# Optimization experiments

Measured on AMD Instinct MI355X. Metric: run time of the kernel, lower is better.

The kernel has to match this reference:

```python
import jax, jax.numpy as jnp
import numpy as np
import math

NUM_LAYERS = 2
D_MODEL = 512
NUM_HEADS = 8
DFF = 2048
TIME_DIM = 8
B = 8
L = 512


def _ffn2(t, w1, b1, w2, b2):
    # gsm_ffn: two Dense(time_dim) layers, both with relu
    h = jax.nn.relu(t @ w1 + b1)
    return jax.nn.relu(h @ w2 + b2)


def _layer_norm(x, g, b, eps=1e-6):
    m = jnp.mean(x, axis=-1, keepdims=True)
    v = jnp.mean(jnp.square(x - m), axis=-1, keepdims=True)
    return (x - m) / jnp.sqrt(v + eps) * g + b


def _forward(x, t, wq, bq, wk, bk, wv, bv, wo, bo, w1, b1, w2, b2,
             ln1g, ln1b, ln2g, ln2b, pw1, pb1, pw2, pb2,
             sw1, sb1, sw2, sb2, bw1, bb1, bw2, bb2):
    Bn, Ln, D = x.shape
    H = NUM_HEADS
    dh = D // H
    scale = jnp.sqrt(jnp.float32(dh))
    two_pi = jnp.float32(2.0 * math.pi)
    for i in range(NUM_LAYERS):
        # ---- TimeGSMKernel: Gibbs spectral-mixture time kernel [B,L,L] ----
        pv = _ffn2(t, pw1[i], pb1[i], pw2[i], pb2[i])            # [B,L,td]
        tp = two_pi * pv * t                                      # [B,L,td]
        cos_enc = jnp.cos(tp[:, :, None, :] - tp[:, None, :, :])  # [B,L,L,td]
        sg = _ffn2(t, sw1[i], sb1[i], sw2[i], sb2[i]) + 1e-6      # [B,L,td]
        sq = sg[:, :, None, :]                                    # [B,L,1,td]
        sk = sg[:, None, :, :]                                    # [B,1,L,td]
        denom = sq * sq + sk * sk
        diff = t[:, :, None, :] - t[:, None, :, :]                # [B,L,L,1]
        exp_enc = jnp.exp(-(diff * diff) / denom)                 # [B,L,L,td]
        local_enc = jnp.sqrt(2.0 * sq * sk / denom)
        be = _ffn2(t, bw1[i], bb1[i], bw2[i], bb2[i])             # [B,L,td]
        kern = jnp.sum(be[:, :, None, :] * be[:, None, :, :]
                       * local_enc * exp_enc * cos_enc, axis=-1)  # [B,L,L]

        # ---- multi-head self-attention with kernel bias ----
        def heads(z):
            return z.reshape(Bn, Ln, H, dh).transpose(0, 2, 1, 3)
        q = heads(x @ wq[i] + bq[i])
        k = heads(x @ wk[i] + bk[i])
        v = heads(x @ wv[i] + bv[i])
        logits = jnp.einsum('bhqd,bhkd->bhqk', q, k) / scale
        logits = logits + (kern / jnp.exp(scale))[:, None, :, :]
        aw = jax.nn.softmax(logits, axis=-1)
        ctx = jnp.einsum('bhqk,bhkd->bhqd', aw, v)
        ctx = ctx.transpose(0, 2, 1, 3).reshape(Bn, Ln, D)
        attn_out = ctx @ wo[i] + bo[i]
        x = _layer_norm(x + attn_out, ln1g[i], ln1b[i])
        # ---- pointwise FFN (relu then linear) ----
        f = jax.nn.relu(x @ w1[i] + b1[i]) @ w2[i] + b2[i]
        x = _layer_norm(x + f, ln2g[i], ln2b[i])
    return x


def setup_inputs() -> dict:
    key = jax.random.key(0)
    ks = iter(jax.random.split(key, 40))
    def nrm(shape, s=0.02):
        return (jax.random.normal(next(ks), shape) * s).astype(jnp.float32)
    NL, D, TD = NUM_LAYERS, D_MODEL, TIME_DIM
    d = {
        'x': jax.random.normal(next(ks), (B, L, D), dtype=jnp.float32),
        't': jax.random.uniform(next(ks), (B, L, 1), dtype=jnp.float32),
        'wq': nrm((NL, D, D)), 'bq': jnp.zeros((NL, D), jnp.float32),
        'wk': nrm((NL, D, D)), 'bk': jnp.zeros((NL, D), jnp.float32),
        'wv': nrm((NL, D, D)), 'bv': jnp.zeros((NL, D), jnp.float32),
        'wo': nrm((NL, D, D)), 'bo': jnp.zeros((NL, D), jnp.float32),
        'w1': nrm((NL, D, DFF)), 'b1': jnp.zeros((NL, DFF), jnp.float32),
        'w2': nrm((NL, DFF, D)), 'b2': jnp.zeros((NL, D), jnp.float32),
        'ln1g': jnp.ones((NL, D), jnp.float32), 'ln1b': jnp.zeros((NL, D), jnp.float32),
        'ln2g': jnp.ones((NL, D), jnp.float32), 'ln2b': jnp.zeros((NL, D), jnp.float32),
        'pw1': nrm((NL, 1, TD), 0.5), 'pb1': 0.1 * jnp.ones((NL, TD), jnp.float32),
        'pw2': nrm((NL, TD, TD), 0.3), 'pb2': 0.1 * jnp.ones((NL, TD), jnp.float32),
        'sw1': nrm((NL, 1, TD), 0.5), 'sb1': 0.1 * jnp.ones((NL, TD), jnp.float32),
        'sw2': nrm((NL, TD, TD), 0.3), 'sb2': 0.5 * jnp.ones((NL, TD), jnp.float32),
        'bw1': nrm((NL, 1, TD), 0.5), 'bb1': 0.1 * jnp.ones((NL, TD), jnp.float32),
        'bw2': nrm((NL, TD, TD), 0.3), 'bb2': 0.1 * jnp.ones((NL, TD), jnp.float32),
    }
    return d


def reference(x, t, wq, bq, wk, bk, wv, bv, wo, bo, w1, b1, w2, b2,
              ln1g, ln1b, ln2g, ln2b, pw1, pb1, pw2, pb2,
              sw1, sb1, sw2, sb2, bw1, bb1, bw2, bb2):
    return _forward(x, t, wq, bq, wk, bk, wv, bv, wo, bo, w1, b1, w2, b2,
                    ln1g, ln1b, ln2g, ln2b, pw1, pb1, pw2, pb2,
                    sw1, sb1, sw2, sb2, bw1, bb1, bw2, bb2)
```

## Files before the change

### kernel.cpp

```cpp
#include <hip/hip_runtime.h>
#include <hip/hip_bf16.h>

#define DEV_INLINE __device__ __forceinline__

constexpr int NLAYERS = 2;
constexpr int DM = 512;
constexpr int NH = 8;
constexpr int DHD = 64;
constexpr int FF = 2048;
constexpr int TD = 8;
constexpr int BB = 8;
constexpr int LL = 512;
constexpr int ROWS = BB * LL;
constexpr int QKVN = 3 * DM;

constexpr float TWO_PI_F = 6.28318530717958647692f;
constexpr float INV_E8 = 3.3546262790251185e-4f;

typedef __attribute__((ext_vector_type(8))) short short8v;
typedef __attribute__((ext_vector_type(4))) float f32x4;

DEV_INLINE unsigned short bf16_rne(float x) {
  unsigned int u = __float_as_uint(x);
  unsigned int r = (u + 0x7fffu + ((u >> 16) & 1u)) >> 16;
  return (unsigned short)r;
}
DEV_INLINE float bf16_to_f(unsigned short h) {
  return __uint_as_float(((unsigned int)h) << 16);
}
DEV_INLINE void split_bf16(float x, unsigned short& h, unsigned short& l) {
  h = bf16_rne(x);
  float lo = x - bf16_to_f(h);
  l = bf16_rne(lo);
}

DEV_INLINE void ffn2_small(float tv,
                           const float* __restrict__ w1, const float* __restrict__ b1,
                           const float* __restrict__ w2, const float* __restrict__ b2,
                           float* out) {
  float h[TD];
#pragma unroll
  for (int d = 0; d < TD; ++d) h[d] = fmaxf(tv * w1[d] + b1[d], 0.f);
#pragma unroll
  for (int j = 0; j < TD; ++j) {
    float acc = b2[j];
#pragma unroll
    for (int d = 0; d < TD; ++d) acc += h[d] * w2[d * TD + j];
    out[j] = fmaxf(acc, 0.f);
  }
}

__global__ __launch_bounds__(256) void small_ffn_kernel(
    const float* __restrict__ t,
    const float* __restrict__ pw1, const float* __restrict__ pb1,
    const float* __restrict__ pw2, const float* __restrict__ pb2,
    const float* __restrict__ sw1, const float* __restrict__ sb1,
    const float* __restrict__ sw2, const float* __restrict__ sb2,
    const float* __restrict__ bw1, const float* __restrict__ bb1,
    const float* __restrict__ bw2, const float* __restrict__ bb2,
    float* __restrict__ tp, float* __restrict__ sg, float* __restrict__ be) {
  const int i = blockIdx.x * 256 + threadIdx.x;
  if (i >= ROWS) return;
  const float tv = t[i];
  float o[TD];
  ffn2_small(tv, pw1, pb1, pw2, pb2, o);
#pragma unroll
  for (int d = 0; d < TD; ++d) tp[(size_t)i * TD + d] = TWO_PI_F * o[d] * tv;
  ffn2_small(tv, sw1, sb1, sw2, sb2, o);
#pragma unroll
  for (int d = 0; d < TD; ++d) sg[(size_t)i * TD + d] = o[d] + 1e-6f;
  ffn2_small(tv, bw1, bb1, bw2, bb2, o);
#pragma unroll
  for (int d = 0; d < TD; ++d) be[(size_t)i * TD + d] = o[d];
}

DEV_INLINE void load8(const float* __restrict__ p, float* o) {
  float4 a = *reinterpret_cast<const float4*>(p);
  float4 b = *reinterpret_cast<const float4*>(p + 4);
  o[0] = a.x; o[1] = a.y; o[2] = a.z; o[3] = a.w;
  o[4] = b.x; o[5] = b.y; o[6] = b.z; o[7] = b.w;
}

__global__ __launch_bounds__(256) void kern_kernel(
    const float* __restrict__ t, const float* __restrict__ tp,
    const float* __restrict__ sg, const float* __restrict__ be,
    float* __restrict__ kernS) {
  const int k = blockIdx.x * 256 + threadIdx.x;
  const int q = blockIdx.y;
  const int b = blockIdx.z;
  const size_t iq = (size_t)b * LL + q;
  const size_t ik = (size_t)b * LL + k;
  const float tq = t[iq], tk = t[ik];
  const float diff = tq - tk;
  const float d2 = diff * diff;

  float tpq[TD], sgq[TD], beq[TD], tpk[TD], sgk[TD], bek[TD];
  load8(tp + iq * TD, tpq);
  load8(sg + iq * TD, sgq);
  load8(be + iq * TD, beq);
  load8(tp + ik * TD, tpk);
  load8(sg + ik * TD, sgk);
  load8(be + ik * TD, bek);

  float acc = 0.f;
#pragma unroll
  for (int d = 0; d < TD; ++d) {
    const float sq = sgq[d], sk = sgk[d];
    const float denom = sq * sq + sk * sk;
    const float inv = 1.0f / denom;
    const float e = __expf(-d2 * inv);
    const float loc = sqrtf(2.0f * sq * sk * inv);
    const float c = __cosf(tpq[d] - tpk[d]);
    acc += beq[d] * bek[d] * loc * e * c;
  }
  kernS[((size_t)b * LL + q) * LL + k] = acc * INV_E8;
}

__global__ __launch_bounds__(256) void td_kernel(
    const float* __restrict__ W, unsigned short* __restrict__ Thi,
    unsigned short* __restrict__ Tlo, int K, int N) {
  __shared__ float tile[32][33];
  const int k0 = blockIdx.x * 32, n0 = blockIdx.y * 32;
  const int tx = threadIdx.x & 31, ty = threadIdx.x >> 5;
#pragma unroll
  for (int i = 0; i < 4; ++i)
    tile[ty + i * 8][tx] = W[(size_t)(k0 + ty + i * 8) * N + n0 + tx];
  __syncthreads();
#pragma unroll
  for (int i = 0; i < 4; ++i) {
    const int n = n0 + ty + i * 8;
    const float v = tile[tx][ty + i * 8];
    unsigned short h, l;
    split_bf16(v, h, l);
    Thi[(size_t)n * K + k0 + tx] = h;
    Tlo[(size_t)n * K + k0 + tx] = l;
  }
}

__global__ __launch_bounds__(256) void decomp_kernel(
    const float* __restrict__ X, unsigned short* __restrict__ Hi,
    unsigned short* __restrict__ Lo, int n4) {
  const int i = blockIdx.x * 256 + threadIdx.x;
  if (i >= n4) return;
  const float4 v = *reinterpret_cast<const float4*>(X + (size_t)i * 4);
  unsigned short h0, h1, h2, h3, l0, l1, l2, l3;
  split_bf16(v.x, h0, l0);
  split_bf16(v.y, h1, l1);
  split_bf16(v.z, h2, l2);
  split_bf16(v.w, h3, l3);
  uint2 hv, lv;
  hv.x = (unsigned)h0 | ((unsigned)h1 << 16);
  hv.y = (unsigned)h2 | ((unsigned)h3 << 16);
  lv.x = (unsigned)l0 | ((unsigned)l1 << 16);
  lv.y = (unsigned)l2 | ((unsigned)l3 << 16);
  *reinterpret_cast<uint2*>(Hi + (size_t)i * 4) = hv;
  *reinterpret_cast<uint2*>(Lo + (size_t)i * 4) = lv;
}

__global__ __launch_bounds__(256) void qkvbias_kernel(
    const float* __restrict__ bq, const float* __restrict__ bk,
    const float* __restrict__ bv, float* __restrict__ out) {
  const int i = blockIdx.x * 256 + threadIdx.x;
  if (i >= QKVN) return;
  out[i] = i < DM ? bq[i] : (i < 2 * DM ? bk[i - DM] : bv[i - 2 * DM]);
}

template <int BN, bool RELU, bool SPLIT_OUT>
__global__ __launch_bounds__(256) void gemm_mfma(
    const unsigned short* __restrict__ Ahi, const unsigned short* __restrict__ Alo,
    const unsigned short* __restrict__ Bhi, const unsigned short* __restrict__ Blo,
    const float* __restrict__ bias, float* __restrict__ C,
    unsigned short* __restrict__ Chi, unsigned short* __restrict__ Clo,
    int M, int N, int K) {
  constexpr int BM = 128, BK = 32;
  constexpr int WT_M = 64;
  constexpr int WT_N = BN / 2;
  constexpr int MI = WT_M / 16;
  constexpr int NI = WT_N / 16;
  constexpr int A_IT = BM * BK / (256 * 8);
  constexpr int B_IT = BN * BK / (256 * 8);

  __shared__ unsigned short AsH[2][BM * BK];
  __shared__ unsigned short AsL[2][BM * BK];
  __shared__ unsigned short BsH[2][BN * BK];
  __shared__ unsigned short BsL[2][BN * BK];

  const int nwg = gridDim.x * gridDim.y;
  const int orig = blockIdx.y * gridDim.x + blockIdx.x;
  const int swz = (orig & 7) * (nwg >> 3) + (orig >> 3);
  const int bx = swz % gridDim.x;
  const int by = swz / gridDim.x;

  const int tid = threadIdx.x;
  const int lane = tid & 63;
  const int wid = tid >> 6;
  const int wr = wid >> 1, wc = wid & 1;
  const int rowBase = by * BM;
  const int colBase = bx * BN;
  const int l15 = lane & 15, l4 = lane >> 4;

  const int sg_ = tid & 3;
  const int srA = tid >> 2;
  const int swg = sg_ ^ (srA & 3) ^ ((srA >> 2) & 3);

  f32x4 acc[MI][NI] = {};
  const int nt = K / BK;

  uint4 ahR[A_IT], alR[A_IT], bhR[B_IT], blR[B_IT];

  auto loadRegs = [&](int kt) {
    const int k0 = kt * BK;
#pragma unroll
    for (int it = 0; it < A_IT; ++it) {
      const size_t base = (size_t)(rowBase + it * 64 + srA) * K + k0 + sg_ * 8;
      ahR[it] = *reinterpret_cast<const uint4*>(Ahi + base);
      alR[it] = *reinterpret_cast<const uint4*>(Alo + base);
    }
#pragma unroll
    for (int it = 0; it < B_IT; ++it) {
      const size_t base = (size_t)(colBase + it * 64 + srA) * K + k0 + sg_ * 8;
      bhR[it] = *reinterpret_cast<const uint4*>(Bhi + base);
      blR[it] = *reinterpret_cast<const uint4*>(Blo + base);
    }
  };

  auto writeLDS = [&](int buf) {
#pragma unroll
    for (int it = 0; it < A_IT; ++it) {
      const int off = ((it * 64 + srA) << 5) + (swg << 3);
      *reinterpret_cast<uint4*>(&AsH[buf][off]) = ahR[it];
      *reinterpret_cast<uint4*>(&AsL[buf][off]) = alR[it];
    }
#pragma unroll
    for (int it = 0; it < B_IT; ++it) {
      const int off = ((it * 64 + srA) << 5) + (swg << 3);
      *reinterpret_cast<uint4*>(&BsH[buf][off]) = bhR[it];
      *reinterpret_cast<uint4*>(&BsL[buf][off]) = blR[it];
    }
  };

  loadRegs(0);
  writeLDS(0);
  if (nt > 1) loadRegs(1);

  for (int t = 0; t < nt; ++t) {
    __syncthreads();
    const int cur = t & 1;
    if (t + 1 < nt) writeLDS(cur ^ 1);
    if (t + 2 < nt) loadRegs(t + 2);

    short8v ah[MI], al[MI], bh[NI], bl[NI];
#pragma unroll
    for (int mi = 0; mi < MI; ++mi) {
      const int r = wr * WT_M + mi * 16 + l15;
      const int g = l4 ^ (r & 3) ^ ((r >> 2) & 3);
      const int off = (r << 5) + (g << 3);
      ah[mi] = *reinterpret_cast<const short8v*>(&AsH[cur][off]);
      al[mi] = *reinterpret_cast<const short8v*>(&AsL[cur][off]);
    }
#pragma unroll
    for (int ni = 0; ni < NI; ++ni) {
      const int r = wc * WT_N + ni * 16 + l15;
      const int g = l4 ^ (r & 3) ^ ((r >> 2) & 3);
      const int off = (r << 5) + (g << 3);
      bh[ni] = *reinterpret_cast<const short8v*>(&BsH[cur][off]);
      bl[ni] = *reinterpret_cast<const short8v*>(&BsL[cur][off]);
    }
#pragma unroll
    for (int mi = 0; mi < MI; ++mi)
#pragma unroll
      for (int ni = 0; ni < NI; ++ni) {
        acc[mi][ni] = __builtin_amdgcn_mfma_f32_16x16x32_bf16(ah[mi], bh[ni], acc[mi][ni], 0, 0, 0);
        acc[mi][ni] = __builtin_amdgcn_mfma_f32_16x16x32_bf16(al[mi], bh[ni], acc[mi][ni], 0, 0, 0);
        acc[mi][ni] = __builtin_amdgcn_mfma_f32_16x16x32_bf16(ah[mi], bl[ni], acc[mi][ni], 0, 0, 0);
      }
  }

#pragma unroll
  for (int mi = 0; mi < MI; ++mi) {
#pragma unroll
    for (int ni = 0; ni < NI; ++ni) {
      const int col = colBase + wc * WT_N + ni * 16 + l15;
      const float bv = bias[col];
#pragma unroll
      for (int j = 0; j < 4; ++j) {
        const int row = rowBase + wr * WT_M + mi * 16 + l4 * 4 + j;
        float v = acc[mi][ni][j] + bv;
        if (RELU) v = fmaxf(v, 0.f);
        if (SPLIT_OUT) {
          unsigned short h, l;
          split_bf16(v, h, l);
          Chi[(size_t)row * N + col] = h;
          Clo[(size_t)row * N + col] = l;
        } else {
          C[(size_t)row * N + col] = v;
        }
      }
    }
  }
}

__global__ __launch_bounds__(256) void vtxp_kernel(
    const unsigned short* __restrict__ qkvhi, const unsigned short* __restrict__ qkvlo,
    unsigned short* __restrict__ vtbhi, unsigned short* __restrict__ vtblo) {
  __shared__ unsigned short th[32][33], tl[32][33];
  const int bh = blockIdx.z;
  const int b = bh >> 3, h = bh & 7;
  const int kk0 = blockIdx.x * 32, d0 = blockIdx.y * 32;
  const int tx = threadIdx.x & 31, ty = threadIdx.x >> 5;
#pragma unroll
  for (int i = 0; i < 4; ++i) {
    const int kk = kk0 + ty + i * 8;
    const size_t src = (size_t)(b * LL + kk) * QKVN + 2 * DM + h * DHD + d0 + tx;
    th[ty + i * 8][tx] = qkvhi[src];
    tl[ty + i * 8][tx] = qkvlo[src];
  }
  __syncthreads();
#pragma unroll
  for (int i = 0; i < 4; ++i) {
    const int d = d0 + ty + i * 8;
    const size_t dst = ((size_t)bh * DHD + d) * LL + kk0 + tx;
    vtbhi[dst] = th[tx][ty + i * 8];
    vtblo[dst] = tl[tx][ty + i * 8];
  }
}

constexpr int ATQ = 16;

__global__ __launch_bounds__(256) void attn_mfma(
    const unsigned short* __restrict__ qkvhi, const unsigned short* __restrict__ qkvlo,
    const unsigned short* __restrict__ vtbhi, const unsigned short* __restrict__ vtblo,
    const float* __restrict__ kernS,
    unsigned short* __restrict__ ctxhi, unsigned short* __restrict__ ctxlo) {
  const int id = blockIdx.x;
  const int w = (id & 7) * 256 + (id >> 3);
  const int h = w & 7;
  const int qt = (w >> 3) & 31;
  const int b = w >> 8;
  const int tid = threadIdx.x;
  const int lane = tid & 63;
  const int wv = tid >> 6;
  const int l15 = lane & 15, l4 = lane >> 4;
  const int q0 = qt * ATQ;

  __shared__ float S[ATQ][521];
  __shared__ unsigned short Phi[ATQ][520];
  __shared__ unsigned short Plo[ATQ][520];
  __shared__ float sinv[ATQ];

  short8v qh[2], ql[2];
  {
    const size_t qbase = (size_t)(b * LL + q0 + l15) * QKVN + h * DHD;
#pragma unroll
    for (int ks = 0; ks < 2; ++ks) {
      qh[ks] = *reinterpret_cast<const short8v*>(qkvhi + qbase + ks * 32 + l4 * 8);
      ql[ks] = *reinterpret_cast<const short8v*>(qkvlo + qbase + ks * 32 + l4 * 8);
    }
  }

  for (int nt = 0; nt < 8; ++nt) {
    const int kk0 = wv * 128 + nt * 16;
    const size_t kbase = (size_t)(b * LL + kk0 + l15) * QKVN + DM + h * DHD;
    f32x4 acc = {};
#pragma unroll
    for (int ks = 0; ks < 2; ++ks) {
      const short8v kh = *reinterpret_cast<const short8v*>(qkvhi + kbase + ks * 32 + l4 * 8);
      const short8v kl = *reinterpret_cast<const short8v*>(qkvlo + kbase + ks * 32 + l4 * 8);
      acc = __builtin_amdgcn_mfma_f32_16x16x32_bf16(qh[ks], kh, acc, 0, 0, 0);
      acc = __builtin_amdgcn_mfma_f32_16x16x32_bf16(ql[ks], kh, acc, 0, 0, 0);
      acc = __builtin_amdgcn_mfma_f32_16x16x32_bf16(qh[ks], kl, acc, 0, 0, 0);
    }
#pragma unroll
    for (int j = 0; j < 4; ++j) {
      const int row = l4 * 4 + j;
      S[row][kk0 + l15] =
          acc[j] * 0.125f + kernS[((size_t)b * LL + q0 + row) * LL + kk0 + l15];
    }
  }
  __syncthreads();

  {
    const int r = tid >> 4, c = tid & 15;
    float m = -1e30f;
#pragma unroll
    for (int j = 0; j < 32; ++j) m = fmaxf(m, S[r][c + j * 16]);
#pragma unroll
    for (int s = 8; s; s >>= 1) m = fmaxf(m, __shfl_xor(m, s, 16));
    float sum = 0.f;
#pragma unroll
    for (int j = 0; j < 32; ++j) {
      const float e = __expf(S[r][c + j * 16] - m);
      unsigned short hh, ll;
      split_bf16(e, hh, ll);
      Phi[r][c + j * 16] = hh;
      Plo[r][c + j * 16] = ll;
      sum += e;
    }
#pragma unroll
    for (int s = 8; s; s >>= 1) sum += __shfl_xor(sum, s, 16);
    if (c == 0) sinv[r] = 1.0f / sum;
  }
  __syncthreads();

  {
    const int d0 = wv * 16;
    const size_t vbase = ((size_t)(b * NH + h) * DHD + d0 + l15) * LL;
    f32x4 acc = {};
    for (int kt = 0; kt < 16; ++kt) {
      const int kk0 = kt * 32;
      const short8v ph = *reinterpret_cast<const short8v*>(&Phi[l15][kk0 + l4 * 8]);
      const short8v pl = *reinterpret_cast<const short8v*>(&Plo[l15][kk0 + l4 * 8]);
      const short8v vh = *reinterpret_cast<const short8v*>(vtbhi + vbase + kk0 + l4 * 8);
      const short8v vl = *reinterpret_cast<const short8v*>(vtblo + vbase + kk0 + l4 * 8);
      acc = __builtin_amdgcn_mfma_f32_16x16x32_bf16(ph, vh, acc, 0, 0, 0);
      acc = __builtin_amdgcn_mfma_f32_16x16x32_bf16(pl, vh, acc, 0, 0, 0);
      acc = __builtin_amdgcn_mfma_f32_16x16x32_bf16(ph, vl, acc, 0, 0, 0);
    }
#pragma unroll
    for (int j = 0; j < 4; ++j) {
      const int row = l4 * 4 + j;
      const float o = acc[j] * sinv[row];
      unsigned short hh, ll;
      split_bf16(o, hh, ll);
      const size_t oo = (size_t)(b * LL + q0 + row) * DM + h * DHD + d0 + l15;
      ctxhi[oo] = hh;
      ctxlo[oo] = ll;
    }
  }
}

__global__ __launch_bounds__(256) void resid_ln_kernel(
    const float* __restrict__ X, const float* __restrict__ R,
    const float* __restrict__ g, const float* __restrict__ bta,
    float* __restrict__ Out, unsigned short* __restrict__ OutHi,
    unsigned short* __restrict__ OutLo) {
  const int row = blockIdx.x * 4 + (threadIdx.x >> 6);
  const int lane = threadIdx.x & 63;
  const float* x = X + (size_t)row * DM;
  const float* r = R + (size_t)row * DM;

  float v[8];
  float s = 0.f;
#pragma unroll
  for (int j = 0; j < 2; ++j) {
    const float4 a = *reinterpret_cast<const float4*>(x + lane * 8 + j * 4);
    const float4 c = *reinterpret_cast<const float4*>(r + lane * 8 + j * 4);
    v[j * 4 + 0] = a.x + c.x;
    v[j * 4 + 1] = a.y + c.y;
    v[j * 4 + 2] = a.z + c.z;
    v[j * 4 + 3] = a.w + c.w;
    s += v[j * 4 + 0] + v[j * 4 + 1] + v[j * 4 + 2] + v[j * 4 + 3];
  }
#pragma unroll
  for (int m = 1; m < 64; m <<= 1) s += __shfl_xor(s, m, 64);
  const float mean = s * (1.f / DM);
  float var = 0.f;
#pragma unroll
  for (int j = 0; j < 8; ++j) {
    const float dlt = v[j] - mean;
    var += dlt * dlt;
  }
#pragma unroll
  for (int m = 1; m < 64; m <<= 1) var += __shfl_xor(var, m, 64);
  var *= (1.f / DM);
  const float inv = 1.0f / sqrtf(var + 1e-6f);

  unsigned short hs[8], ls[8];
#pragma unroll
  for (int j = 0; j < 2; ++j) {
    const float4 gg = *reinterpret_cast<const float4*>(g + lane * 8 + j * 4);
    const float4 bb = *reinterpret_cast<const float4*>(bta + lane * 8 + j * 4);
    float4 o;
    o.x = (v[j * 4 + 0] - mean) * inv * gg.x + bb.x;
    o.y = (v[j * 4 + 1] - mean) * inv * gg.y + bb.y;
    o.z = (v[j * 4 + 2] - mean) * inv * gg.z + bb.z;
    o.w = (v[j * 4 + 3] - mean) * inv * gg.w + bb.w;
    *reinterpret_cast<float4*>(Out + (size_t)row * DM + lane * 8 + j * 4) = o;
    split_bf16(o.x, hs[j * 4 + 0], ls[j * 4 + 0]);
    split_bf16(o.y, hs[j * 4 + 1], ls[j * 4 + 1]);
    split_bf16(o.z, hs[j * 4 + 2], ls[j * 4 + 2]);
    split_bf16(o.w, hs[j * 4 + 3], ls[j * 4 + 3]);
  }
  uint4 hv, lv;
  hv.x = (unsigned)hs[0] | ((unsigned)hs[1] << 16);
  hv.y = (unsigned)hs[2] | ((unsigned)hs[3] << 16);
  hv.z = (unsigned)hs[4] | ((unsigned)hs[5] << 16);
  hv.w = (unsigned)hs[6] | ((unsigned)hs[7] << 16);
  lv.x = (unsigned)ls[0] | ((unsigned)ls[1] << 16);
  lv.y = (unsigned)ls[2] | ((unsigned)ls[3] << 16);
  lv.z = (unsigned)ls[4] | ((unsigned)ls[5] << 16);
  lv.w = (unsigned)ls[6] | ((unsigned)ls[7] << 16);
  *reinterpret_cast<uint4*>(OutHi + (size_t)row * DM + lane * 8) = hv;
  *reinterpret_cast<uint4*>(OutLo + (size_t)row * DM + lane * 8) = lv;
}

extern "C" void kernel_launch(void* const* d_in, const int* in_sizes, int n_in,
                              void* d_out, int out_size, void* d_ws, size_t ws_size,
                              hipStream_t stream) {
  const float* x_in = (const float*)d_in[0];
  const float* t = (const float*)d_in[1];
  const float* wq = (const float*)d_in[2];
  const float* bq = (const float*)d_in[3];
  const float* wk = (const float*)d_in[4];
  const float* bk = (const float*)d_in[5];
  const float* wv = (const float*)d_in[6];
  const float* bv = (const float*)d_in[7];
  const float* wo = (const float*)d_in[8];
  const float* bo = (const float*)d_in[9];
  const float* w1 = (const float*)d_in[10];
  const float* b1 = (const float*)d_in[11];
  const float* w2 = (const float*)d_in[12];
  const float* b2 = (const float*)d_in[13];
  const float* ln1g = (const float*)d_in[14];
  const float* ln1b = (const float*)d_in[15];
  const float* ln2g = (const float*)d_in[16];
  const float* ln2b = (const float*)d_in[17];
  const float* pw1 = (const float*)d_in[18];
  const float* pb1 = (const float*)d_in[19];
  const float* pw2 = (const float*)d_in[20];
  const float* pb2 = (const float*)d_in[21];
  const float* sw1 = (const float*)d_in[22];
  const float* sb1 = (const float*)d_in[23];
  const float* sw2 = (const float*)d_in[24];
  const float* sb2 = (const float*)d_in[25];
  const float* bw1 = (const float*)d_in[26];
  const float* bb1 = (const float*)d_in[27];
  const float* bw2 = (const float*)d_in[28];
  const float* bb2 = (const float*)d_in[29];

  char* wsb = (char*)d_ws;
  size_t off = 0;
  auto allocB = [&](size_t bytes) {
    char* p = wsb + off;
    off += (bytes + 255) & ~(size_t)255;
    return p;
  };
  float* tpb = (float*)allocB(ROWS * TD * 4);
  float* sgb = (float*)allocB(ROWS * TD * 4);
  float* beb = (float*)allocB(ROWS * TD * 4);
  float* kernS = (float*)allocB((size_t)BB * LL * LL * 4);
  unsigned short* qkvhi = (unsigned short*)allocB(
      ((size_t)ROWS * QKVN * 2 + (size_t)BB * NH * DHD * LL * 2) * 2);
  unsigned short* qkvlo = qkvhi + (size_t)ROWS * QKVN;
  unsigned short* vtbhi = qkvlo + (size_t)ROWS * QKVN;
  unsigned short* vtblo = vtbhi + (size_t)BB * NH * DHD * LL;
  float* ao = (float*)allocB((size_t)ROWS * DM * 4);
  float* xb = (float*)allocB((size_t)ROWS * DM * 4);
  float* fb = (float*)allocB((size_t)ROWS * DM * 4);
  float* xn = (float*)allocB((size_t)ROWS * DM * 4);
  float* qkvbias = (float*)allocB(QKVN * 4);
  unsigned short* qkvwt_hi = (unsigned short*)allocB((size_t)QKVN * DM * 2);
  unsigned short* qkvwt_lo = (unsigned short*)allocB((size_t)QKVN * DM * 2);
  unsigned short* wot_hi = (unsigned short*)allocB((size_t)DM * DM * 2);
  unsigned short* wot_lo = (unsigned short*)allocB((size_t)DM * DM * 2);
  unsigned short* w1t_hi = (unsigned short*)allocB((size_t)FF * DM * 2);
  unsigned short* w1t_lo = (unsigned short*)allocB((size_t)FF * DM * 2);
  unsigned short* w2t_hi = (unsigned short*)allocB((size_t)DM * FF * 2);
  unsigned short* w2t_lo = (unsigned short*)allocB((size_t)DM * FF * 2);
  unsigned short* xhi = (unsigned short*)allocB((size_t)ROWS * DM * 2);
  unsigned short* xlo = (unsigned short*)allocB((size_t)ROWS * DM * 2);
  unsigned short* ctxhi = (unsigned short*)allocB((size_t)ROWS * DM * 2);
  unsigned short* ctxlo = (unsigned short*)allocB((size_t)ROWS * DM * 2);
  unsigned short* hhi = qkvhi;
  unsigned short* hlo = hhi + (size_t)ROWS * FF;

  const float* xcur = x_in;

  for (int i = 0; i < NLAYERS; ++i) {
    td_kernel<<<dim3(16, 16), 256, 0, stream>>>(wq + (size_t)i * DM * DM, qkvwt_hi, qkvwt_lo, DM, DM);
    td_kernel<<<dim3(16, 16), 256, 0, stream>>>(wk + (size_t)i * DM * DM, qkvwt_hi + (size_t)DM * DM, qkvwt_lo + (size_t)DM * DM, DM, DM);
    td_kernel<<<dim3(16, 16), 256, 0, stream>>>(wv + (size_t)i * DM * DM, qkvwt_hi + (size_t)2 * DM * DM, qkvwt_lo + (size_t)2 * DM * DM, DM, DM);
    td_kernel<<<dim3(16, 16), 256, 0, stream>>>(wo + (size_t)i * DM * DM, wot_hi, wot_lo, DM, DM);
    td_kernel<<<dim3(16, 64), 256, 0, stream>>>(w1 + (size_t)i * DM * FF, w1t_hi, w1t_lo, DM, FF);
    td_kernel<<<dim3(64, 16), 256, 0, stream>>>(w2 + (size_t)i * FF * DM, w2t_hi, w2t_lo, FF, DM);
    qkvbias_kernel<<<(QKVN + 255) / 256, 256, 0, stream>>>(bq + i * DM, bk + i * DM, bv + i * DM, qkvbias);

    small_ffn_kernel<<<ROWS / 256, 256, 0, stream>>>(
        t, pw1 + i * TD, pb1 + i * TD, pw2 + i * TD * TD, pb2 + i * TD,
        sw1 + i * TD, sb1 + i * TD, sw2 + i * TD * TD, sb2 + i * TD,
        bw1 + i * TD, bb1 + i * TD, bw2 + i * TD * TD, bb2 + i * TD,
        tpb, sgb, beb);
    kern_kernel<<<dim3(LL / 256, LL, BB), 256, 0, stream>>>(t, tpb, sgb, beb, kernS);

    if (i == 0) {
      decomp_kernel<<<(ROWS * DM / 4 + 255) / 256, 256, 0, stream>>>(x_in, xhi, xlo, ROWS * DM / 4);
    }

    gemm_mfma<128, false, true><<<dim3(QKVN / 128, ROWS / 128), 256, 0, stream>>>(
        xhi, xlo, qkvwt_hi, qkvwt_lo, qkvbias, nullptr, qkvhi, qkvlo, ROWS, QKVN, DM);

    vtxp_kernel<<<dim3(LL / 32, DHD / 32, BB * NH), 256, 0, stream>>>(
        qkvhi, qkvlo, vtbhi, vtblo);

    attn_mfma<<<dim3(BB * NH * (LL / ATQ)), 256, 0, stream>>>(
        qkvhi, qkvlo, vtbhi, vtblo, kernS, ctxhi, ctxlo);

    gemm_mfma<64, false, false><<<dim3(DM / 64, ROWS / 128), 256, 0, stream>>>(
        ctxhi, ctxlo, wot_hi, wot_lo, bo + i * DM, ao, nullptr, nullptr, ROWS, DM, DM);

    resid_ln_kernel<<<ROWS / 4, 256, 0, stream>>>(
        xcur, ao, ln1g + i * DM, ln1b + i * DM, xb, xhi, xlo);

    gemm_mfma<128, true, true><<<dim3(FF / 128, ROWS / 128), 256, 0, stream>>>(
        xhi, xlo, w1t_hi, w1t_lo, b1 + i * FF, nullptr, hhi, hlo, ROWS, FF, DM);

    gemm_mfma<64, false, false><<<dim3(DM / 64, ROWS / 128), 256, 0, stream>>>(
        hhi, hlo, w2t_hi, w2t_lo, b2 + i * DM, fb, nullptr, nullptr, ROWS, DM, FF);

    float* ln2_out = (i == NLAYERS - 1) ? (float*)d_out : xn;
    resid_ln_kernel<<<ROWS / 4, 256, 0, stream>>>(
        xb, fb, ln2g + i * DM, ln2b + i * DM, ln2_out, xhi, xlo);

    xcur = xn;
  }
}
```

Measured before the change: 851.2 us.

## Shrink GEMM row tiles to 64 and split-K the FFN down-projection

Makes the GEMM row tile a template parameter and launches all four GEMMs with 64-row tiles instead of 128, doubling the workgroup count so the 256 CUs of the MI355X are better occupied. The FFN second GEMM (K=2048, N=512) is also split along K into two partial outputs, which a new reduction kernel sums together with the bias. This is meant to fix under-filled grids on narrow-N GEMMs. In exchange, smaller tiles give less operand reuse per block, and the split-K path adds extra global traffic for the partial buffers plus one more launch.

```diff
diff --git a/kernel.cpp b/kernel.cpp
--- a/kernel.cpp
+++ b/kernel.cpp
@@ -165,15 +165,15 @@
   out[i] = i < DM ? bq[i] : (i < 2 * DM ? bk[i - DM] : bv[i - 2 * DM]);
 }
 
-template <int BN, bool RELU, bool SPLIT_OUT>
+template <int BM, int BN, bool RELU, bool SPLIT_OUT, bool PARTIAL>
 __global__ __launch_bounds__(256) void gemm_mfma(
     const unsigned short* __restrict__ Ahi, const unsigned short* __restrict__ Alo,
     const unsigned short* __restrict__ Bhi, const unsigned short* __restrict__ Blo,
     const float* __restrict__ bias, float* __restrict__ C,
     unsigned short* __restrict__ Chi, unsigned short* __restrict__ Clo,
     int M, int N, int K) {
-  constexpr int BM = 128, BK = 32;
-  constexpr int WT_M = 64;
+  constexpr int BK = 32;
+  constexpr int WT_M = BM / 2;
   constexpr int WT_N = BN / 2;
   constexpr int MI = WT_M / 16;
   constexpr int NI = WT_N / 16;
@@ -203,13 +203,16 @@
   const int srA = tid >> 2;
   const int swg = sg_ ^ (srA & 3) ^ ((srA >> 2) & 3);
 
+  const int Keff = K / gridDim.z;
+  const int koff = blockIdx.z * Keff;
+
   f32x4 acc[MI][NI] = {};
-  const int nt = K / BK;
+  const int nt = Keff / BK;
 
   uint4 ahR[A_IT], alR[A_IT], bhR[B_IT], blR[B_IT];
 
   auto loadRegs = [&](int kt) {
-    const int k0 = kt * BK;
+    const int k0 = koff + kt * BK;
 #pragma unroll
     for (int it = 0; it < A_IT; ++it) {
       const size_t base = (size_t)(rowBase + it * 64 + srA) * K + k0 + sg_ * 8;
@@ -276,12 +279,13 @@
       }
   }
 
+  float* Cout = PARTIAL ? (C + (size_t)blockIdx.z * M * N) : C;
 #pragma unroll
   for (int mi = 0; mi < MI; ++mi) {
 #pragma unroll
     for (int ni = 0; ni < NI; ++ni) {
       const int col = colBase + wc * WT_N + ni * 16 + l15;
-      const float bv = bias[col];
+      const float bv = PARTIAL ? 0.f : bias[col];
 #pragma unroll
       for (int j = 0; j < 4; ++j) {
         const int row = rowBase + wr * WT_M + mi * 16 + l4 * 4 + j;
@@ -293,11 +297,29 @@
           Chi[(size_t)row * N + col] = h;
           Clo[(size_t)row * N + col] = l;
         } else {
-          C[(size_t)row * N + col] = v;
+          Cout[(size_t)row * N + col] = v;
         }
       }
     }
   }
+}
+
+__global__ __launch_bounds__(256) void redk_kernel(
+    const float* __restrict__ part, const float* __restrict__ bias,
+    float* __restrict__ out, int total4, int N) {
+  const int i = blockIdx.x * 256 + threadIdx.x;
+  if (i >= total4) return;
+  const size_t idx = (size_t)i * 4;
+  const int col = (int)(idx & (N - 1));
+  const float4 a = *reinterpret_cast<const float4*>(part + idx);
+  const float4 b = *reinterpret_cast<const float4*>(part + (size_t)ROWS * DM + idx);
+  const float4 bi = *reinterpret_cast<const float4*>(bias + col);
+  float4 o;
+  o.x = a.x + b.x + bi.x;
+  o.y = a.y + b.y + bi.y;
+  o.z = a.z + b.z + bi.z;
+  o.w = a.w + b.w + bi.w;
+  *reinterpret_cast<float4*>(out + idx) = o;
 }
 
 __global__ __launch_bounds__(256) void vtxp_kernel(
@@ -548,6 +570,7 @@
   float* xb = (float*)allocB((size_t)ROWS * DM * 4);
   float* fb = (float*)allocB((size_t)ROWS * DM * 4);
   float* xn = (float*)allocB((size_t)ROWS * DM * 4);
+  float* part = (float*)allocB((size_t)2 * ROWS * DM * 4);
   float* qkvbias = (float*)allocB(QKVN * 4);
   unsigned short* qkvwt_hi = (unsigned short*)allocB((size_t)QKVN * DM * 2);
   unsigned short* qkvwt_lo = (unsigned short*)allocB((size_t)QKVN * DM * 2);
@@ -586,7 +609,7 @@
       decomp_kernel<<<(ROWS * DM / 4 + 255) / 256, 256, 0, stream>>>(x_in, xhi, xlo, ROWS * DM / 4);
     }
 
-    gemm_mfma<128, false, true><<<dim3(QKVN / 128, ROWS / 128), 256, 0, stream>>>(
+    gemm_mfma<64, 128, false, true, false><<<dim3(QKVN / 128, ROWS / 64), 256, 0, stream>>>(
         xhi, xlo, qkvwt_hi, qkvwt_lo, qkvbias, nullptr, qkvhi, qkvlo, ROWS, QKVN, DM);
 
     vtxp_kernel<<<dim3(LL / 32, DHD / 32, BB * NH), 256, 0, stream>>>(
@@ -595,17 +618,19 @@
     attn_mfma<<<dim3(BB * NH * (LL / ATQ)), 256, 0, stream>>>(
         qkvhi, qkvlo, vtbhi, vtblo, kernS, ctxhi, ctxlo);
 
-    gemm_mfma<64, false, false><<<dim3(DM / 64, ROWS / 128), 256, 0, stream>>>(
+    gemm_mfma<64, 64, false, false, false><<<dim3(DM / 64, ROWS / 64), 256, 0, stream>>>(
         ctxhi, ctxlo, wot_hi, wot_lo, bo + i * DM, ao, nullptr, nullptr, ROWS, DM, DM);
 
     resid_ln_kernel<<<ROWS / 4, 256, 0, stream>>>(
         xcur, ao, ln1g + i * DM, ln1b + i * DM, xb, xhi, xlo);
 
-    gemm_mfma<128, true, true><<<dim3(FF / 128, ROWS / 128), 256, 0, stream>>>(
+    gemm_mfma<64, 128, true, true, false><<<dim3(FF / 128, ROWS / 64), 256, 0, stream>>>(
         xhi, xlo, w1t_hi, w1t_lo, b1 + i * FF, nullptr, hhi, hlo, ROWS, FF, DM);
 
-    gemm_mfma<64, false, false><<<dim3(DM / 64, ROWS / 128), 256, 0, stream>>>(
-        hhi, hlo, w2t_hi, w2t_lo, b2 + i * DM, fb, nullptr, nullptr, ROWS, DM, FF);
+    gemm_mfma<64, 64, false, false, true><<<dim3(DM / 64, ROWS / 64, 2), 256, 0, stream>>>(
+        hhi, hlo, w2t_hi, w2t_lo, nullptr, part, nullptr, nullptr, ROWS, DM, FF);
+    redk_kernel<<<(ROWS * DM / 4 + 255) / 256, 256, 0, stream>>>(
+        part, b2 + i * DM, fb, ROWS * DM / 4, DM);
 
     float* ln2_out = (i == NLAYERS - 1) ? (float*)d_out : xn;
     resid_ln_kernel<<<ROWS / 4, 256, 0, stream>>>(
```

Result: faster. 797.3 us (-6.3%).
